# Kernel optimization log

Measured on AMD Instinct MI355X. Metric: run time of the kernel, lower is better.

## Reference

```python
import jax, jax.numpy as jnp
import numpy as np

T, B, DIM_IN, DIM_STATE, NUM_CLASSES = 256, 64, 256, 512, 10000


def setup_inputs() -> dict:
    key = jax.random.key(0)
    ks = jax.random.split(key, 6)
    inputs = jax.random.normal(ks[0], (T, B, DIM_IN), dtype=jnp.float32)
    labels = jax.random.uniform(ks[1], (T, B, NUM_CLASSES), dtype=jnp.float32)
    labels = labels / jnp.sum(labels, axis=-1, keepdims=True)  # soft label distributions
    initial_state = jnp.zeros((B, DIM_STATE), dtype=jnp.float32)
    initial_output = jnp.zeros((B, DIM_STATE), dtype=jnp.float32)
    # LSTM cell params: gates packed as [i, f, g, o]
    Wx = jax.random.normal(ks[2], (DIM_IN, 4 * DIM_STATE), dtype=jnp.float32) * (1.0 / np.sqrt(DIM_IN))
    Wh = jax.random.normal(ks[3], (DIM_STATE, 4 * DIM_STATE), dtype=jnp.float32) * (1.0 / np.sqrt(DIM_STATE))
    b = jnp.zeros((4 * DIM_STATE,), dtype=jnp.float32)
    # Final FC (softmax head) params
    Wo = jax.random.normal(ks[4], (DIM_STATE, NUM_CLASSES), dtype=jnp.float32) * (1.0 / np.sqrt(DIM_STATE))
    bo = jnp.zeros((NUM_CLASSES,), dtype=jnp.float32)
    return {"inputs": inputs, "labels": labels, "initial_state": initial_state,
            "initial_output": initial_output, "Wx": Wx, "Wh": Wh, "b": b, "Wo": Wo, "bo": bo}


def reference(inputs, labels, initial_state, initial_output, Wx, Wh, b, Wo, bo):
    def step(carry, x_t):
        h, c = carry  # h: [B, DIM_STATE] previous output; c: [B, DIM_STATE] cell state
        z = x_t @ Wx + h @ Wh + b  # [B, 4*DIM_STATE]
        i, f, g, o = jnp.split(z, 4, axis=-1)
        c = jax.nn.sigmoid(f) * c + jax.nn.sigmoid(i) * jnp.tanh(g)
        h = jax.nn.sigmoid(o) * jnp.tanh(c)
        return (h, c), h

    _, hs = jax.lax.scan(step, (initial_output, initial_state), inputs)  # hs: [T, B, DIM_STATE]
    logits = jnp.einsum('tbs,sc->tbc', hs, Wo) + bo  # [T, B, NUM_CLASSES]
    log_p = jax.nn.log_softmax(logits, axis=-1)
    predictions = jnp.exp(log_p)  # softmax probabilities
    # softmax_cross_entropy_with_logits per (t, b), then mean over all
    total_loss = -jnp.mean(jnp.sum(labels * log_p, axis=-1))
    return predictions, total_loss
```

## Files before the change

kernel.cpp:

```cpp
#include <hip/hip_runtime.h>
#include <hip/hip_bf16.h>
#include <math.h>

#define T_STEPS 256
#define BATCH 64
#define DIN 256
#define DSTATE 512
#define NGATE 2048
#define NCLS 10000
#define NCLS_PAD 10112
#define ROWS 16384
#define SCAN_BLOCKS 64
#define CHUNK_ROWS 4096

typedef __attribute__((ext_vector_type(8))) short bf16x8;
typedef __attribute__((ext_vector_type(4))) float f32x4;

__device__ inline unsigned short f2b(float x) {
    __hip_bfloat16 h = __float2bfloat16(x);
    return *(unsigned short*)&h;
}
__device__ inline float b2f(unsigned short u) {
    return __uint_as_float(((unsigned int)u) << 16);
}


__global__ void init_bar(unsigned* __restrict__ bar) {
    bar[threadIdx.x] = 0u;
}

__global__ void f32_to_bf16(const float* __restrict__ in, unsigned short* __restrict__ out, int n4) {
    int i = blockIdx.x * 256 + threadIdx.x;
    if (i >= n4) return;
    float4 v = *(const float4*)&in[i * 4];
    ushort4 o;
    o.x = f2b(v.x); o.y = f2b(v.y); o.z = f2b(v.z); o.w = f2b(v.w);
    *(ushort4*)&out[i * 4] = o;
}

__global__ void build_wT(const float* __restrict__ W, unsigned short* __restrict__ WT,
                         int kshift, int total) {
    int e = blockIdx.x * 256 + threadIdx.x;
    if (e >= total) return;
    int jp = e >> kshift;
    int k = e & ((1 << kshift) - 1);
    int s = jp >> 2, g = jp & 3;
    WT[e] = f2b(W[(size_t)k * NGATE + g * DSTATE + s]);
}

__global__ void build_bias(const float* __restrict__ b, float* __restrict__ bp) {
    int jp = blockIdx.x * 256 + threadIdx.x;
    if (jp >= NGATE) return;
    bp[jp] = b[(jp & 3) * DSTATE + (jp >> 2)];
}

__launch_bounds__(256)
__global__ void transpose_wo(const float* __restrict__ Wo, unsigned short* __restrict__ WoT) {
    __shared__ float tile[64][65];
    const int tid = threadIdx.x;
    const int n0 = blockIdx.x * 64, k0 = blockIdx.y * 64;
    #pragma unroll
    for (int r = 0; r < 16; ++r) {
        int k = (tid >> 6) + r * 4;
        int n = tid & 63;
        float v = (n0 + n < NCLS) ? Wo[(size_t)(k0 + k) * NCLS + n0 + n] : 0.f;
        tile[k][n] = v;
    }
    __syncthreads();
    #pragma unroll
    for (int r = 0; r < 16; ++r) {
        int n = (tid >> 6) + r * 4;
        int k = tid & 63;
        WoT[(size_t)(n0 + n) * DSTATE + k0 + k] = f2b(tile[k][n]);
    }
}

__launch_bounds__(256)
__global__ void zx_gemm(const unsigned short* __restrict__ Xb,
                        const unsigned short* __restrict__ WxT,
                        const float* __restrict__ bp,
                        unsigned short* __restrict__ ZxT) {
    __shared__ unsigned short As[64][264];
    __shared__ unsigned short Bs[128][264];
    __shared__ float zls[4][32][65];
    const int tid = threadIdx.x;
    const int t = blockIdx.x;
    const int n0 = blockIdx.y * 128;
    const int wave = tid >> 6, lane = tid & 63, mr = lane & 15, g = lane >> 4;

    #pragma unroll
    for (int r = 0; r < 8; ++r) {
        int c = r * 256 + tid; int row = c >> 5, q = c & 31;
        *(int4*)&As[row][q * 8] = *(const int4*)&Xb[((size_t)t * 64 + row) * DIN + q * 8];
    }
    #pragma unroll
    for (int r = 0; r < 16; ++r) {
        int c = r * 256 + tid; int row = c >> 5, q = c & 31;
        *(int4*)&Bs[row][q * 8] = *(const int4*)&WxT[(size_t)(n0 + row) * DIN + q * 8];
    }
    __syncthreads();

    f32x4 acc[4][2] = {};
    #pragma unroll
    for (int kt = 0; kt < DIN; kt += 32) {
        bf16x8 af[4], bf[2];
        #pragma unroll
        for (int fm = 0; fm < 4; ++fm) af[fm] = *(const bf16x8*)&As[fm * 16 + mr][kt + g * 8];
        #pragma unroll
        for (int fn = 0; fn < 2; ++fn) bf[fn] = *(const bf16x8*)&Bs[wave * 32 + fn * 16 + mr][kt + g * 8];
        #pragma unroll
        for (int fm = 0; fm < 4; ++fm)
            #pragma unroll
            for (int fn = 0; fn < 2; ++fn)
                acc[fm][fn] = __builtin_amdgcn_mfma_f32_16x16x32_bf16(af[fm], bf[fn], acc[fm][fn], 0, 0, 0);
    }
    #pragma unroll
    for (int fm = 0; fm < 4; ++fm)
        #pragma unroll
        for (int fn = 0; fn < 2; ++fn)
            #pragma unroll
            for (int r = 0; r < 4; ++r)
                zls[wave][fn * 16 + mr][fm * 16 + g * 4 + r] = acc[fm][fn][r];
    #pragma unroll 4
    for (int jr = 0; jr < 32; ++jr) {
        int j = n0 + wave * 32 + jr;
        float v = zls[wave][jr][lane] + bp[j];
        ZxT[((size_t)t * NGATE + j) * 64 + lane] = f2b(v);
    }
}

__device__ __forceinline__ void gridbar(unsigned* cnt, unsigned* flg, unsigned want, int tid) {
    __syncthreads();
    if (tid == 0) {
        unsigned old = __hip_atomic_fetch_add(cnt, 1u, __ATOMIC_ACQ_REL, __HIP_MEMORY_SCOPE_AGENT);
        if (old == SCAN_BLOCKS - 1) {
            __hip_atomic_store(cnt, 0u, __ATOMIC_RELAXED, __HIP_MEMORY_SCOPE_AGENT);
            __hip_atomic_store(flg, want, __ATOMIC_RELEASE, __HIP_MEMORY_SCOPE_AGENT);
        } else {
            while (__hip_atomic_load(flg, __ATOMIC_RELAXED, __HIP_MEMORY_SCOPE_AGENT) < want) {}
            (void)__hip_atomic_load(flg, __ATOMIC_ACQUIRE, __HIP_MEMORY_SCOPE_AGENT);
        }
    }
    __syncthreads();
}

__launch_bounds__(256, 1)
__global__ void lstm_scan_mfma(const unsigned short* __restrict__ h0b,
                               const float* __restrict__ c0,
                               const unsigned short* __restrict__ WhT,
                               const unsigned short* __restrict__ ZxT,
                               unsigned short* __restrict__ hsb,
                               unsigned* __restrict__ bar) {
    __shared__ unsigned short Wl[32][520];
    __shared__ unsigned short hT[64][520];
    __shared__ float zb[64][33];
    const int tid = threadIdx.x;
    const int bid = blockIdx.x;
    const int j0 = bid * 32;
    const int s0 = bid * 8;
    const int wave = tid >> 6, lane = tid & 63, mr = lane & 15, g = lane >> 4;
    unsigned* bcnt = bar;
    unsigned* bflg = bar + 32;

    #pragma unroll
    for (int r = 0; r < 8; ++r) {
        int c = r * 256 + tid; int row = c >> 6, q = c & 63;
        *(int4*)&Wl[row][q * 8] = *(const int4*)&WhT[(size_t)(j0 + row) * DSTATE + q * 8];
    }

    const int gb = tid >> 2;
    const int sl0 = (tid & 3) * 2;
    float creg0 = c0[gb * DSTATE + s0 + sl0];
    float creg1 = c0[gb * DSTATE + s0 + sl0 + 1];
    __syncthreads();

    const size_t zo0 = ((size_t)(j0 + mr)) * 64 + wave * 16 + g * 4;
    const size_t zo1 = ((size_t)(j0 + 16 + mr)) * 64 + wave * 16 + g * 4;
    ushort4 za0 = *(const ushort4*)&ZxT[zo0];
    ushort4 za1 = *(const ushort4*)&ZxT[zo1];

    for (int t = 0; t < T_STEPS; ++t) {
        const unsigned short* hsrc = t ? (hsb + (size_t)(t - 1) * BATCH * DSTATE) : h0b;
        #pragma unroll
        for (int r = 0; r < 16; ++r) {
            int c = r * 256 + tid; int row = c >> 6, q = c & 63;
            *(int4*)&hT[row][q * 8] = *(const int4*)&hsrc[(size_t)row * DSTATE + q * 8];
        }
        __syncthreads();

        f32x4 acc0, acc1;
        acc0[0] = b2f(za0.x); acc0[1] = b2f(za0.y); acc0[2] = b2f(za0.z); acc0[3] = b2f(za0.w);
        acc1[0] = b2f(za1.x); acc1[1] = b2f(za1.y); acc1[2] = b2f(za1.z); acc1[3] = b2f(za1.w);
        if (t + 1 < T_STEPS) {
            za0 = *(const ushort4*)&ZxT[(size_t)(t + 1) * NGATE * 64 + zo0];
            za1 = *(const ushort4*)&ZxT[(size_t)(t + 1) * NGATE * 64 + zo1];
        }
        #pragma unroll
        for (int kt = 0; kt < DSTATE; kt += 32) {
            bf16x8 af = *(const bf16x8*)&hT[wave * 16 + mr][kt + g * 8];
            acc0 = __builtin_amdgcn_mfma_f32_16x16x32_bf16(af, *(const bf16x8*)&Wl[mr][kt + g * 8], acc0, 0, 0, 0);
            acc1 = __builtin_amdgcn_mfma_f32_16x16x32_bf16(af, *(const bf16x8*)&Wl[16 + mr][kt + g * 8], acc1, 0, 0, 0);
        }
        #pragma unroll
        for (int r = 0; r < 4; ++r) {
            zb[wave * 16 + g * 4 + r][mr] = acc0[r];
            zb[wave * 16 + g * 4 + r][16 + mr] = acc1[r];
        }
        {
            float zi0 = zb[gb][sl0 * 4 + 0], zf0 = zb[gb][sl0 * 4 + 1];
            float zg0 = zb[gb][sl0 * 4 + 2], zo0v = zb[gb][sl0 * 4 + 3];
            float zi1 = zb[gb][sl0 * 4 + 4], zf1 = zb[gb][sl0 * 4 + 5];
            float zg1 = zb[gb][sl0 * 4 + 6], zo1v = zb[gb][sl0 * 4 + 7];
            float i0 = 1.f / (1.f + expf(-zi0)), f0 = 1.f / (1.f + expf(-zf0));
            float o0 = 1.f / (1.f + expf(-zo0v)), g0 = tanhf(zg0);
            float i1 = 1.f / (1.f + expf(-zi1)), f1 = 1.f / (1.f + expf(-zf1));
            float o1 = 1.f / (1.f + expf(-zo1v)), g1 = tanhf(zg1);
            creg0 = f0 * creg0 + i0 * g0;
            creg1 = f1 * creg1 + i1 * g1;
            float h0v = o0 * tanhf(creg0);
            float h1v = o1 * tanhf(creg1);
            ushort2 hv; hv.x = f2b(h0v); hv.y = f2b(h1v);
            *(ushort2*)&hsb[((size_t)t * BATCH + gb) * DSTATE + s0 + sl0] = hv;
        }
        if (t != T_STEPS - 1)
            gridbar(bcnt, bflg, (unsigned)(t + 1), tid);
    }
}

__launch_bounds__(256)
__global__ void gemm_logits_bf16(const unsigned short* __restrict__ A,
                                 const unsigned short* __restrict__ Bt,
                                 const float* __restrict__ bo,
                                 unsigned short* __restrict__ Cb) {
    __shared__ unsigned short As[128 * 32];
    __shared__ unsigned short Bs[128 * 32];
    const int tid = threadIdx.x;
    const int wave = tid >> 6, lane = tid & 63;
    const int wm = wave >> 1, wn = wave & 1;
    const int m0 = blockIdx.y * 128, n0 = blockIdx.x * 128;
    const int g = lane >> 4, mr = lane & 15;

    const int ch0 = wave * 64 + lane;
    const int ch1 = (4 + wave) * 64 + lane;
    const int row0 = ch0 >> 2, q0 = ch0 & 3;
    const int row1 = ch1 >> 2, q1 = ch1 & 3;

    f32x4 acc[4][4] = {};
    for (int kt = 0; kt < DSTATE; kt += 32) {
        __builtin_amdgcn_global_load_lds(
            (const __attribute__((address_space(1))) void*)&A[(size_t)(m0 + row0) * DSTATE + kt + q0 * 8],
            (__attribute__((address_space(3))) void*)&As[ch0 * 8 - lane * 8], 16, 0, 0);
        __builtin_amdgcn_global_load_lds(
            (const __attribute__((address_space(1))) void*)&A[(size_t)(m0 + row1) * DSTATE + kt + q1 * 8],
            (__attribute__((address_space(3))) void*)&As[ch1 * 8 - lane * 8], 16, 0, 0);
        __builtin_amdgcn_global_load_lds(
            (const __attribute__((address_space(1))) void*)&Bt[(size_t)(n0 + row0) * DSTATE + kt + q0 * 8],
            (__attribute__((address_space(3))) void*)&Bs[ch0 * 8 - lane * 8], 16, 0, 0);
        __builtin_amdgcn_global_load_lds(
            (const __attribute__((address_space(1))) void*)&Bt[(size_t)(n0 + row1) * DSTATE + kt + q1 * 8],
            (__attribute__((address_space(3))) void*)&Bs[ch1 * 8 - lane * 8], 16, 0, 0);
        __syncthreads();

        bf16x8 af[4], bf[4];
        #pragma unroll
        for (int f = 0; f < 4; ++f) {
            af[f] = *(const bf16x8*)&As[(wm * 64 + f * 16 + mr) * 32 + g * 8];
            bf[f] = *(const bf16x8*)&Bs[(wn * 64 + f * 16 + mr) * 32 + g * 8];
        }
        #pragma unroll
        for (int fm = 0; fm < 4; ++fm)
            #pragma unroll
            for (int fn = 0; fn < 4; ++fn)
                acc[fm][fn] = __builtin_amdgcn_mfma_f32_16x16x32_bf16(af[fm], bf[fn], acc[fm][fn], 0, 0, 0);
        __syncthreads();
    }
    #pragma unroll
    for (int fm = 0; fm < 4; ++fm) {
        #pragma unroll
        for (int fn = 0; fn < 4; ++fn) {
            int col = n0 + wn * 64 + fn * 16 + mr;
            if (col >= NCLS) continue;
            float bias = bo[col];
            #pragma unroll
            for (int r = 0; r < 4; ++r) {
                int row = m0 + wm * 64 + fm * 16 + g * 4 + r;
                Cb[(size_t)row * NCLS + col] = f2b(acc[fm][fn][r] + bias);
            }
        }
    }
}

__launch_bounds__(256)
__global__ void gemm_logits_mfma(const unsigned short* __restrict__ A,
                                 const unsigned short* __restrict__ Bt,
                                 const float* __restrict__ bo,
                                 float* __restrict__ C) {
    __shared__ unsigned short As[128 * 32];
    __shared__ unsigned short Bs[128 * 32];
    const int tid = threadIdx.x;
    const int wave = tid >> 6, lane = tid & 63;
    const int wm = wave >> 1, wn = wave & 1;
    const int m0 = blockIdx.y * 128, n0 = blockIdx.x * 128;
    const int g = lane >> 4, mr = lane & 15;

    const int ch0 = wave * 64 + lane;
    const int ch1 = (4 + wave) * 64 + lane;
    const int row0 = ch0 >> 2, q0 = ch0 & 3;
    const int row1 = ch1 >> 2, q1 = ch1 & 3;

    f32x4 acc[4][4] = {};
    for (int kt = 0; kt < DSTATE; kt += 32) {
        __builtin_amdgcn_global_load_lds(
            (const __attribute__((address_space(1))) void*)&A[(size_t)(m0 + row0) * DSTATE + kt + q0 * 8],
            (__attribute__((address_space(3))) void*)&As[ch0 * 8 - lane * 8], 16, 0, 0);
        __builtin_amdgcn_global_load_lds(
            (const __attribute__((address_space(1))) void*)&A[(size_t)(m0 + row1) * DSTATE + kt + q1 * 8],
            (__attribute__((address_space(3))) void*)&As[ch1 * 8 - lane * 8], 16, 0, 0);
        __builtin_amdgcn_global_load_lds(
            (const __attribute__((address_space(1))) void*)&Bt[(size_t)(n0 + row0) * DSTATE + kt + q0 * 8],
            (__attribute__((address_space(3))) void*)&Bs[ch0 * 8 - lane * 8], 16, 0, 0);
        __builtin_amdgcn_global_load_lds(
            (const __attribute__((address_space(1))) void*)&Bt[(size_t)(n0 + row1) * DSTATE + kt + q1 * 8],
            (__attribute__((address_space(3))) void*)&Bs[ch1 * 8 - lane * 8], 16, 0, 0);
        __syncthreads();

        bf16x8 af[4], bf[4];
        #pragma unroll
        for (int f = 0; f < 4; ++f) {
            af[f] = *(const bf16x8*)&As[(wm * 64 + f * 16 + mr) * 32 + g * 8];
            bf[f] = *(const bf16x8*)&Bs[(wn * 64 + f * 16 + mr) * 32 + g * 8];
        }
        #pragma unroll
        for (int fm = 0; fm < 4; ++fm)
            #pragma unroll
            for (int fn = 0; fn < 4; ++fn)
                acc[fm][fn] = __builtin_amdgcn_mfma_f32_16x16x32_bf16(af[fm], bf[fn], acc[fm][fn], 0, 0, 0);
        __syncthreads();
    }
    #pragma unroll
    for (int fm = 0; fm < 4; ++fm) {
        #pragma unroll
        for (int fn = 0; fn < 4; ++fn) {
            int col = n0 + wn * 64 + fn * 16 + mr;
            if (col >= NCLS) continue;
            float bias = bo[col];
            #pragma unroll
            for (int r = 0; r < 4; ++r) {
                int row = m0 + wm * 64 + fm * 16 + g * 4 + r;
                C[(size_t)row * NCLS + col] = acc[fm][fn][r] + bias;
            }
        }
    }
}

__device__ inline float wave_reduce_max(float v) {
    #pragma unroll
    for (int off = 32; off > 0; off >>= 1) v = fmaxf(v, __shfl_xor(v, off));
    return v;
}
__device__ inline float wave_reduce_sum(float v) {
    #pragma unroll
    for (int off = 32; off > 0; off >>= 1) v += __shfl_xor(v, off);
    return v;
}

__launch_bounds__(256)
__global__ void softmax_loss_bf16(const unsigned short* __restrict__ Cb,
                                  const float* __restrict__ labels,
                                  float* __restrict__ probs,
                                  float* __restrict__ rowloss) {
    __shared__ float row[NCLS];
    __shared__ float sm[4];
    const int tid = threadIdx.x;
    const size_t base = (size_t)blockIdx.x * NCLS;

    float m = -INFINITY;
    for (int c8 = tid; c8 < NCLS / 8; c8 += 256) {
        ushort4 u0 = *(const ushort4*)&Cb[base + c8 * 8];
        ushort4 u1 = *(const ushort4*)&Cb[base + c8 * 8 + 4];
        float v0 = b2f(u0.x), v1 = b2f(u0.y), v2 = b2f(u0.z), v3 = b2f(u0.w);
        float v4 = b2f(u1.x), v5 = b2f(u1.y), v6 = b2f(u1.z), v7 = b2f(u1.w);
        float4 a = {v0, v1, v2, v3}, b = {v4, v5, v6, v7};
        *(float4*)&row[c8 * 8] = a;
        *(float4*)&row[c8 * 8 + 4] = b;
        m = fmaxf(m, fmaxf(fmaxf(fmaxf(v0, v1), fmaxf(v2, v3)),
                           fmaxf(fmaxf(v4, v5), fmaxf(v6, v7))));
    }
    m = wave_reduce_max(m);
    if ((tid & 63) == 0) sm[tid >> 6] = m;
    __syncthreads();
    m = fmaxf(fmaxf(sm[0], sm[1]), fmaxf(sm[2], sm[3]));
    __syncthreads();

    float s = 0.f, dot = 0.f;
    for (int c4 = tid; c4 < NCLS / 4; c4 += 256) {
        float4 v = *(const float4*)&row[c4 * 4];
        float4 lb = *(const float4*)&labels[base + c4 * 4];
        s += expf(v.x - m) + expf(v.y - m) + expf(v.z - m) + expf(v.w - m);
        dot += lb.x * v.x + lb.y * v.y + lb.z * v.z + lb.w * v.w;
    }
    s = wave_reduce_sum(s);
    if ((tid & 63) == 0) sm[tid >> 6] = s;
    __syncthreads();
    s = sm[0] + sm[1] + sm[2] + sm[3];
    __syncthreads();
    dot = wave_reduce_sum(dot);
    if ((tid & 63) == 0) sm[tid >> 6] = dot;
    __syncthreads();
    dot = sm[0] + sm[1] + sm[2] + sm[3];

    float inv = 1.f / s;
    for (int c4 = tid; c4 < NCLS / 4; c4 += 256) {
        float4 v = *(const float4*)&row[c4 * 4];
        float4 o;
        o.x = expf(v.x - m) * inv; o.y = expf(v.y - m) * inv;
        o.z = expf(v.z - m) * inv; o.w = expf(v.w - m) * inv;
        *(float4*)&probs[base + c4 * 4] = o;
    }
    if (tid == 0) rowloss[blockIdx.x] = (m + logf(s)) - dot;
}

__launch_bounds__(256)
__global__ void softmax_loss(float* __restrict__ logits,
                             const float* __restrict__ labels,
                             float* __restrict__ rowloss) {
    __shared__ float row[NCLS];
    __shared__ float sm[4];
    const int tid = threadIdx.x;
    const size_t base = (size_t)blockIdx.x * NCLS;

    float m = -INFINITY;
    for (int c4 = tid; c4 < NCLS / 4; c4 += 256) {
        float4 v = *(const float4*)&logits[base + c4 * 4];
        *(float4*)&row[c4 * 4] = v;
        m = fmaxf(fmaxf(m, fmaxf(v.x, v.y)), fmaxf(v.z, v.w));
    }
    m = wave_reduce_max(m);
    if ((tid & 63) == 0) sm[tid >> 6] = m;
    __syncthreads();
    m = fmaxf(fmaxf(sm[0], sm[1]), fmaxf(sm[2], sm[3]));
    __syncthreads();

    float s = 0.f, dot = 0.f;
    for (int c4 = tid; c4 < NCLS / 4; c4 += 256) {
        float4 v = *(const float4*)&row[c4 * 4];
        float4 lb = *(const float4*)&labels[base + c4 * 4];
        s += expf(v.x - m) + expf(v.y - m) + expf(v.z - m) + expf(v.w - m);
        dot += lb.x * v.x + lb.y * v.y + lb.z * v.z + lb.w * v.w;
    }
    s = wave_reduce_sum(s);
    if ((tid & 63) == 0) sm[tid >> 6] = s;
    __syncthreads();
    s = sm[0] + sm[1] + sm[2] + sm[3];
    __syncthreads();
    dot = wave_reduce_sum(dot);
    if ((tid & 63) == 0) sm[tid >> 6] = dot;
    __syncthreads();
    dot = sm[0] + sm[1] + sm[2] + sm[3];

    float inv = 1.f / s;
    for (int c4 = tid; c4 < NCLS / 4; c4 += 256) {
        float4 v = *(const float4*)&row[c4 * 4];
        float4 o;
        o.x = expf(v.x - m) * inv; o.y = expf(v.y - m) * inv;
        o.z = expf(v.z - m) * inv; o.w = expf(v.w - m) * inv;
        *(float4*)&logits[base + c4 * 4] = o;
    }
    if (tid == 0) rowloss[blockIdx.x] = (m + logf(s)) - dot;
}

__launch_bounds__(256)
__global__ void loss_reduce(const float* __restrict__ rowloss, float* __restrict__ out) {
    __shared__ float sm[4];
    float s = 0.f;
    for (int i = threadIdx.x; i < ROWS; i += 256) s += rowloss[i];
    s = wave_reduce_sum(s);
    if ((threadIdx.x & 63) == 0) sm[threadIdx.x >> 6] = s;
    __syncthreads();
    if (threadIdx.x == 0) out[0] = (sm[0] + sm[1] + sm[2] + sm[3]) * (1.f / ROWS);
}

extern "C" void kernel_launch(void* const* d_in, const int* in_sizes, int n_in,
                              void* d_out, int out_size, void* d_ws, size_t ws_size,
                              hipStream_t stream) {
    const float* inputs = (const float*)d_in[0];
    const float* labels = (const float*)d_in[1];
    const float* c0     = (const float*)d_in[2];
    const float* h0     = (const float*)d_in[3];
    const float* Wx     = (const float*)d_in[4];
    const float* Wh     = (const float*)d_in[5];
    const float* bias   = (const float*)d_in[6];
    const float* Wo     = (const float*)d_in[7];
    const float* bo     = (const float*)d_in[8];
    float* out = (float*)d_out;

    float* ws = (float*)d_ws;
    float* bp       = ws;
    float* rowloss  = bp + 2048;
    unsigned short* WhT = (unsigned short*)(rowloss + 16384);
    unsigned short* WxT = WhT + 1048576;
    unsigned short* Xb  = WxT + 524288;
    unsigned short* h0b = Xb + 4194304;
    unsigned short* hsb = h0b + 32768;
    unsigned short* WoT = hsb + 8388608;
    unsigned short* ZxT = WoT + 5177344;
    unsigned* bar = (unsigned*)(ZxT + 33554432);
    unsigned short* Cb = (unsigned short*)(bar + 64);

    size_t base_bytes = (size_t)((char*)Cb - (char*)d_ws);
    size_t need_bf16 = base_bytes + (size_t)CHUNK_ROWS * NCLS * sizeof(unsigned short);
    bool use_bf16 = (ws_size >= need_bf16);

    init_bar<<<1, 64, 0, stream>>>(bar);
    f32_to_bf16<<<(ROWS * DIN / 4 + 255) / 256, 256, 0, stream>>>(inputs, Xb, ROWS * DIN / 4);
    f32_to_bf16<<<(BATCH * DSTATE / 4 + 255) / 256, 256, 0, stream>>>(h0, h0b, BATCH * DSTATE / 4);
    build_wT<<<(NGATE * DSTATE + 255) / 256, 256, 0, stream>>>(Wh, WhT, 9, NGATE * DSTATE);
    build_wT<<<(NGATE * DIN + 255) / 256, 256, 0, stream>>>(Wx, WxT, 8, NGATE * DIN);
    build_bias<<<(NGATE + 255) / 256, 256, 0, stream>>>(bias, bp);
    transpose_wo<<<dim3(NCLS_PAD / 64, DSTATE / 64), 256, 0, stream>>>(Wo, WoT);

    zx_gemm<<<dim3(T_STEPS, NGATE / 128), 256, 0, stream>>>(Xb, WxT, bp, ZxT);

    void* args[] = {(void*)&h0b, (void*)&c0, (void*)&WhT, (void*)&ZxT, (void*)&hsb, (void*)&bar};
    hipLaunchCooperativeKernel((const void*)lstm_scan_mfma, dim3(SCAN_BLOCKS), dim3(256),
                               args, 0, stream);

    if (use_bf16) {
        for (int row0 = 0; row0 < ROWS; row0 += CHUNK_ROWS) {
            gemm_logits_bf16<<<dim3(NCLS_PAD / 128, CHUNK_ROWS / 128), 256, 0, stream>>>(
                hsb + (size_t)row0 * DSTATE, WoT, bo, Cb);
            softmax_loss_bf16<<<CHUNK_ROWS, 256, 0, stream>>>(
                Cb, labels + (size_t)row0 * NCLS, out + (size_t)row0 * NCLS, rowloss + row0);
        }
    } else {
        gemm_logits_mfma<<<dim3(NCLS_PAD / 128, ROWS / 128), 256, 0, stream>>>(hsb, WoT, bo, out);
        softmax_loss<<<ROWS, 256, 0, stream>>>(out, labels, rowloss);
    }
    loss_reduce<<<1, 256, 0, stream>>>(rowloss, out + (size_t)ROWS * NCLS);
}
```

Measured before the change: 2.281 ms.

## Split LSTM scan into independent batch groups with per-group barriers

Repartitions the recurrent scan so each group of 16 blocks owns 16 batch rows and the full hidden dimension. Each block holds a 128-gate slice of Wh in LDS. Because batch rows are independent, synchronisation becomes a barrier over 16 blocks per group instead of a grid-wide barrier over all 64, and each block reads only its 16 rows of h per step. In exchange, each block holds four times as much of Wh in LDS, and the same weight slice is duplicated across the four groups.

```diff
diff --git a/kernel.cpp b/kernel.cpp
--- a/kernel.cpp
+++ b/kernel.cpp
@@ -11,6 +11,7 @@
 #define NCLS_PAD 10112
 #define ROWS 16384
 #define SCAN_BLOCKS 64
+#define GROUP_BLOCKS 16
 #define CHUNK_ROWS 4096
 
 typedef __attribute__((ext_vector_type(8))) short bf16x8;
@@ -129,11 +130,11 @@
     }
 }
 
-__device__ __forceinline__ void gridbar(unsigned* cnt, unsigned* flg, unsigned want, int tid) {
+__device__ __forceinline__ void groupbar(unsigned* cnt, unsigned* flg, unsigned want, int tid) {
     __syncthreads();
     if (tid == 0) {
         unsigned old = __hip_atomic_fetch_add(cnt, 1u, __ATOMIC_ACQ_REL, __HIP_MEMORY_SCOPE_AGENT);
-        if (old == SCAN_BLOCKS - 1) {
+        if (old == GROUP_BLOCKS - 1) {
             __hip_atomic_store(cnt, 0u, __ATOMIC_RELAXED, __HIP_MEMORY_SCOPE_AGENT);
             __hip_atomic_store(flg, want, __ATOMIC_RELEASE, __HIP_MEMORY_SCOPE_AGENT);
         } else {
@@ -151,40 +152,43 @@
                                const unsigned short* __restrict__ ZxT,
                                unsigned short* __restrict__ hsb,
                                unsigned* __restrict__ bar) {
-    __shared__ unsigned short Wl[32][520];
-    __shared__ unsigned short hT[64][520];
-    __shared__ float zb[64][33];
+    __shared__ unsigned short Wl[128][520];
+    __shared__ unsigned short hT[16][520];
+    __shared__ float zb[16][132];
     const int tid = threadIdx.x;
     const int bid = blockIdx.x;
-    const int j0 = bid * 32;
-    const int s0 = bid * 8;
-    const int wave = tid >> 6, lane = tid & 63, mr = lane & 15, g = lane >> 4;
-    unsigned* bcnt = bar;
-    unsigned* bflg = bar + 32;
-
-    #pragma unroll
-    for (int r = 0; r < 8; ++r) {
+    const int grp = bid >> 4;
+    const int w   = bid & 15;
+    const int b0  = grp * 16;
+    const int j0  = w * 128;
+    const int s0  = w * 32;
+    const int wave = tid >> 6, lane = tid & 63, mr = lane & 15, gl = lane >> 4;
+    unsigned* bcnt = bar + grp * 64;
+    unsigned* bflg = bar + grp * 64 + 32;
+
+    #pragma unroll 4
+    for (int r = 0; r < 32; ++r) {
         int c = r * 256 + tid; int row = c >> 6, q = c & 63;
         *(int4*)&Wl[row][q * 8] = *(const int4*)&WhT[(size_t)(j0 + row) * DSTATE + q * 8];
     }
 
-    const int gb = tid >> 2;
-    const int sl0 = (tid & 3) * 2;
-    float creg0 = c0[gb * DSTATE + s0 + sl0];
-    float creg1 = c0[gb * DSTATE + s0 + sl0 + 1];
-    __syncthreads();
-
-    const size_t zo0 = ((size_t)(j0 + mr)) * 64 + wave * 16 + g * 4;
-    const size_t zo1 = ((size_t)(j0 + 16 + mr)) * 64 + wave * 16 + g * 4;
+    const int gb  = lane >> 2;
+    const int slg = wave * 8 + (lane & 3) * 2;
+    float creg0 = c0[(b0 + gb) * DSTATE + s0 + slg];
+    float creg1 = c0[(b0 + gb) * DSTATE + s0 + slg + 1];
+    __syncthreads();
+
+    const size_t zo0 = ((size_t)(j0 + wave * 32 + mr)) * 64 + b0 + gl * 4;
+    const size_t zo1 = ((size_t)(j0 + wave * 32 + 16 + mr)) * 64 + b0 + gl * 4;
     ushort4 za0 = *(const ushort4*)&ZxT[zo0];
     ushort4 za1 = *(const ushort4*)&ZxT[zo1];
 
     for (int t = 0; t < T_STEPS; ++t) {
         const unsigned short* hsrc = t ? (hsb + (size_t)(t - 1) * BATCH * DSTATE) : h0b;
         #pragma unroll
-        for (int r = 0; r < 16; ++r) {
+        for (int r = 0; r < 4; ++r) {
             int c = r * 256 + tid; int row = c >> 6, q = c & 63;
-            *(int4*)&hT[row][q * 8] = *(const int4*)&hsrc[(size_t)row * DSTATE + q * 8];
+            *(int4*)&hT[row][q * 8] = *(const int4*)&hsrc[(size_t)(b0 + row) * DSTATE + q * 8];
         }
         __syncthreads();
 
@@ -197,20 +201,20 @@
         }
         #pragma unroll
         for (int kt = 0; kt < DSTATE; kt += 32) {
-            bf16x8 af = *(const bf16x8*)&hT[wave * 16 + mr][kt + g * 8];
-            acc0 = __builtin_amdgcn_mfma_f32_16x16x32_bf16(af, *(const bf16x8*)&Wl[mr][kt + g * 8], acc0, 0, 0, 0);
-            acc1 = __builtin_amdgcn_mfma_f32_16x16x32_bf16(af, *(const bf16x8*)&Wl[16 + mr][kt + g * 8], acc1, 0, 0, 0);
+            bf16x8 af = *(const bf16x8*)&hT[mr][kt + gl * 8];
+            acc0 = __builtin_amdgcn_mfma_f32_16x16x32_bf16(af, *(const bf16x8*)&Wl[wave * 32 + mr][kt + gl * 8], acc0, 0, 0, 0);
+            acc1 = __builtin_amdgcn_mfma_f32_16x16x32_bf16(af, *(const bf16x8*)&Wl[wave * 32 + 16 + mr][kt + gl * 8], acc1, 0, 0, 0);
         }
         #pragma unroll
         for (int r = 0; r < 4; ++r) {
-            zb[wave * 16 + g * 4 + r][mr] = acc0[r];
-            zb[wave * 16 + g * 4 + r][16 + mr] = acc1[r];
+            zb[gl * 4 + r][wave * 32 + mr] = acc0[r];
+            zb[gl * 4 + r][wave * 32 + 16 + mr] = acc1[r];
         }
         {
-            float zi0 = zb[gb][sl0 * 4 + 0], zf0 = zb[gb][sl0 * 4 + 1];
-            float zg0 = zb[gb][sl0 * 4 + 2], zo0v = zb[gb][sl0 * 4 + 3];
-            float zi1 = zb[gb][sl0 * 4 + 4], zf1 = zb[gb][sl0 * 4 + 5];
-            float zg1 = zb[gb][sl0 * 4 + 6], zo1v = zb[gb][sl0 * 4 + 7];
+            float zi0 = zb[gb][slg * 4 + 0], zf0 = zb[gb][slg * 4 + 1];
+            float zg0 = zb[gb][slg * 4 + 2], zo0v = zb[gb][slg * 4 + 3];
+            float zi1 = zb[gb][slg * 4 + 4], zf1 = zb[gb][slg * 4 + 5];
+            float zg1 = zb[gb][slg * 4 + 6], zo1v = zb[gb][slg * 4 + 7];
             float i0 = 1.f / (1.f + expf(-zi0)), f0 = 1.f / (1.f + expf(-zf0));
             float o0 = 1.f / (1.f + expf(-zo0v)), g0 = tanhf(zg0);
             float i1 = 1.f / (1.f + expf(-zi1)), f1 = 1.f / (1.f + expf(-zf1));
@@ -220,10 +224,10 @@
             float h0v = o0 * tanhf(creg0);
             float h1v = o1 * tanhf(creg1);
             ushort2 hv; hv.x = f2b(h0v); hv.y = f2b(h1v);
-            *(ushort2*)&hsb[((size_t)t * BATCH + gb) * DSTATE + s0 + sl0] = hv;
+            *(ushort2*)&hsb[((size_t)t * BATCH + b0 + gb) * DSTATE + s0 + slg] = hv;
         }
         if (t != T_STEPS - 1)
-            gridbar(bcnt, bflg, (unsigned)(t + 1), tid);
+            groupbar(bcnt, bflg, (unsigned)(t + 1), tid);
     }
 }
 
@@ -505,13 +509,13 @@
     unsigned short* WoT = hsb + 8388608;
     unsigned short* ZxT = WoT + 5177344;
     unsigned* bar = (unsigned*)(ZxT + 33554432);
-    unsigned short* Cb = (unsigned short*)(bar + 64);
+    unsigned short* Cb = (unsigned short*)(bar + 256);
 
     size_t base_bytes = (size_t)((char*)Cb - (char*)d_ws);
     size_t need_bf16 = base_bytes + (size_t)CHUNK_ROWS * NCLS * sizeof(unsigned short);
     bool use_bf16 = (ws_size >= need_bf16);
 
-    init_bar<<<1, 64, 0, stream>>>(bar);
+    init_bar<<<1, 256, 0, stream>>>(bar);
     f32_to_bf16<<<(ROWS * DIN / 4 + 255) / 256, 256, 0, stream>>>(inputs, Xb, ROWS * DIN / 4);
     f32_to_bf16<<<(BATCH * DSTATE / 4 + 255) / 256, 256, 0, stream>>>(h0, h0b, BATCH * DSTATE / 4);
     build_wT<<<(NGATE * DSTATE + 255) / 256, 256, 0, stream>>>(Wh, WhT, 9, NGATE * DSTATE);
```

Result: faster. 2.009 ms (-11.9%).
